# Optimization experiments

Hardware: AMD Instinct MI355X
Metric: run time of the kernel (lower is better)

## Reference

```python
import jax, jax.numpy as jnp
import numpy as np

N = 100000
E = 1600000
EPS = 1e-5


def _bn(h, g, b):
    # BatchNorm1d in training mode: batch stats over dim 0 (biased variance)
    mu = h.mean(0)
    var = ((h - mu) ** 2).mean(0)
    return g * (h - mu) * jax.lax.rsqrt(var + EPS) + b


def setup_inputs() -> dict:
    key = jax.random.key(0)

    def nrm(i, shape, scale=1.0):
        return jax.random.normal(jax.random.fold_in(key, i), shape, jnp.float32) * scale

    inp = {
        "x": nrm(0, (N, 1)),
        "edge_attr": nrm(1, (E, 2)),
        "edge_index": jax.random.randint(jax.random.fold_in(key, 2), (2, E), 0, N),
        "dir_edge_index": jax.random.randint(jax.random.fold_in(key, 3), (2, E), 0, N),
        "prop_edge_index": jax.random.randint(jax.random.fold_in(key, 4), (2, E), 0, N),
    }
    k = [10]

    def lin(name, fan_in, fan_out):
        inp[name] = nrm(k[0], (fan_in, fan_out), 1.0 / float(np.sqrt(fan_in)))
        k[0] += 1

    def bnp(prefix, c):
        inp[prefix + "_g"] = jnp.ones((c,), jnp.float32)
        inp[prefix + "_b"] = jnp.zeros((c,), jnp.float32)

    lin("c1_ws", 1, 2); lin("c1_wn", 1, 2); lin("c1_we", 2, 2); bnp("c1", 2)
    lin("d1_ws", 3, 4); lin("d1_wn", 3, 4); bnp("d1", 4)
    lin("c2_ws", 5, 6); lin("c2_wn", 5, 6); lin("c2_we", 2, 6); bnp("c2", 6)
    lin("d2_ws", 7, 8); lin("d2_wn", 7, 8); bnp("d2", 8)
    lin("c3_ws", 9, 10); lin("c3_wn", 9, 10); lin("c3_we", 2, 10); bnp("c3", 10)
    lin("d3_ws", 11, 12); lin("d3_wn", 11, 12); bnp("d3", 12)
    lin("pw1", 13, 8); inp["pb1"] = jnp.zeros((8,), jnp.float32); bnp("p1", 8)
    lin("pw2", 8, 4); inp["pb2"] = jnp.zeros((4,), jnp.float32); bnp("p2", 4)
    lin("pw3", 4, 1); inp["pb3"] = jnp.zeros((1,), jnp.float32)
    lin("ew1", 28, 14); inp["eb1"] = jnp.zeros((14,), jnp.float32); bnp("e1", 14)
    lin("ew2", 14, 1); inp["eb2"] = jnp.zeros((1,), jnp.float32)
    return inp


def reference(x, edge_attr, edge_index, dir_edge_index, prop_edge_index,
              c1_ws, c1_wn, c1_we, c1_g, c1_b,
              d1_ws, d1_wn, d1_g, d1_b,
              c2_ws, c2_wn, c2_we, c2_g, c2_b,
              d2_ws, d2_wn, d2_g, d2_b,
              c3_ws, c3_wn, c3_we, c3_g, c3_b,
              d3_ws, d3_wn, d3_g, d3_b,
              pw1, pb1, p1_g, p1_b, pw2, pb2, p2_g, p2_b, pw3, pb3,
              ew1, eb1, e1_g, e1_b, ew2, eb2):
    n = x.shape[0]
    src, dst = edge_index[0], edge_index[1]        # x_j = x[src], x_i = x[dst]
    psrc, pdst = prop_edge_index[0], prop_edge_index[1]

    def flexconv(h, ws, wn, we, g, b):
        m = jax.nn.relu(_bn(h[dst] @ ws + edge_attr @ we + h[src] @ wn, g, b))
        agg = jax.ops.segment_sum(m, dst, num_segments=n)
        return jnp.concatenate([h[:, :1], agg], axis=1)

    def edgeinter(h, ws, wn, g, b):
        m = jax.nn.relu(_bn(h[pdst] @ ws + h[psrc] @ wn, g, b))
        agg = jax.ops.segment_sum(m, pdst, num_segments=n)
        return jnp.concatenate([h[:, :1], agg], axis=1)

    out = flexconv(x, c1_ws, c1_wn, c1_we, c1_g, c1_b)      # [N,3]
    out = edgeinter(out, d1_ws, d1_wn, d1_g, d1_b)          # [N,5]
    out = flexconv(out, c2_ws, c2_wn, c2_we, c2_g, c2_b)    # [N,7]
    out = edgeinter(out, d2_ws, d2_wn, d2_g, d2_b)          # [N,9]
    out = flexconv(out, c3_ws, c3_wn, c3_we, c3_g, c3_b)    # [N,11]
    out = edgeinter(out, d3_ws, d3_wn, d3_g, d3_b)          # [N,13]

    h = _bn(jax.nn.relu(out @ pw1 + pb1), p1_g, p1_b)
    h = _bn(jax.nn.relu(h @ pw2 + pb2), p2_g, p2_b)
    power = jax.nn.sigmoid(1.5 * (h @ pw3 + pb3))           # [N,1]

    dsrc, ddst = dir_edge_index[0], dir_edge_index[1]
    f = jnp.concatenate([out[ddst], power[ddst], out[dsrc], power[dsrc]], axis=1)  # [E,28]
    e = _bn(jax.nn.relu(f @ ew1 + eb1), e1_g, e1_b)
    direction = jax.nn.sigmoid(1.5 * (e @ ew2 + eb2))       # [E,1]
    return power, direction
```

## Files before the change

kernel.cpp:

```cpp
#include <hip/hip_runtime.h>
#include <hip/hip_fp16.h>
#include <math.h>

static constexpr int BLK = 256;
static constexpr float BN_EPS = 1e-5f;

__device__ __forceinline__ float sigmoid15(float z) {
    return 1.0f / (1.0f + expf(-1.5f * z));
}

__device__ __forceinline__ unsigned pack_ea(float2 v) {
    unsigned hx = __half_as_ushort(__float2half_rn(v.x));
    unsigned hy = __half_as_ushort(__float2half_rn(v.y));
    return hx | (hy << 16);
}
__device__ __forceinline__ float2 unpack_ea(unsigned u) {
    return make_float2(__half2float(__ushort_as_half((unsigned short)(u & 0xffffu))),
                       __half2float(__ushort_as_half((unsigned short)(u >> 16))));
}

template<int C>
__device__ __forceinline__ void block_stats_reduce(float (&s)[C], float (&ss)[C],
                                                   double* __restrict__ stats)
{
    #pragma unroll
    for (int j = 0; j < C; ++j) {
        #pragma unroll
        for (int o = 32; o > 0; o >>= 1) {
            s[j]  += __shfl_down(s[j],  o, 64);
            ss[j] += __shfl_down(ss[j], o, 64);
        }
    }
    __shared__ float red[2][C][BLK / 64];
    const int wave = threadIdx.x >> 6, lane = threadIdx.x & 63;
    if (lane == 0) {
        #pragma unroll
        for (int j = 0; j < C; ++j) { red[0][j][wave] = s[j]; red[1][j][wave] = ss[j]; }
    }
    __syncthreads();
    if (threadIdx.x < C) {
        const int j = threadIdx.x;
        float a = 0.f, b = 0.f;
        #pragma unroll
        for (int w = 0; w < BLK / 64; ++w) { a += red[0][j][w]; b += red[1][j][w]; }
        atomicAdd(&stats[j],      (double)a);
        atomicAdd(&stats[16 + j], (double)b);
    }
}

template<int C>
__device__ __forceinline__ void bn_coefs(const double* __restrict__ stats,
                                         const float* __restrict__ g, const float* __restrict__ b,
                                         double invE, float (&sc)[C], float (&bb)[C])
{
    #pragma unroll
    for (int j = 0; j < C; ++j) {
        const double mu  = stats[j] * invE;
        const double var = stats[16 + j] * invE - mu * mu;
        const float inv = rsqrtf((float)(var + (double)BN_EPS));
        const float gg = g[j];
        sc[j] = gg * inv;
        bb[j] = b[j] - (float)mu * gg * inv;
    }
}


__global__ __launch_bounds__(BLK) void init_kernel(int* __restrict__ deg, double* __restrict__ stats,
                                                   int* __restrict__ rowstart, int n2, int total)
{
    const int i = blockIdx.x * blockDim.x + threadIdx.x;
    if (i < n2) deg[i] = 0;
    if (i < 288) stats[i] = 0.0;
    if (i == 0) rowstart[n2] = total;
}

__global__ __launch_bounds__(BLK) void hist_kernel(const int* __restrict__ edst,
                                                   const int* __restrict__ pdst,
                                                   int* __restrict__ deg, int N, int E)
{
    const int stride = gridDim.x * blockDim.x;
    for (int e = blockIdx.x * blockDim.x + threadIdx.x; e < E; e += stride) {
        atomicAdd(&deg[edst[e]], 1);
        atomicAdd(&deg[N + pdst[e]], 1);
    }
}

__global__ __launch_bounds__(256) void scan1_kernel(const int* __restrict__ deg,
                                                    int* __restrict__ rowstart,
                                                    int* __restrict__ partials, int n2)
{
    __shared__ int lds[256];
    const int tid = threadIdx.x;
    const int base = blockIdx.x * 1024 + tid * 4;
    int v[4]; int loc = 0;
    #pragma unroll
    for (int r = 0; r < 4; ++r) { v[r] = (base + r < n2) ? deg[base + r] : 0; loc += v[r]; }
    lds[tid] = loc; __syncthreads();
    #pragma unroll
    for (int off = 1; off < 256; off <<= 1) {
        int t = (tid >= off) ? lds[tid - off] : 0;
        __syncthreads();
        lds[tid] += t;
        __syncthreads();
    }
    int excl = lds[tid] - loc;
    int run = excl;
    #pragma unroll
    for (int r = 0; r < 4; ++r) {
        if (base + r < n2) rowstart[base + r] = run;
        run += v[r];
    }
    if (tid == 255) partials[blockIdx.x] = lds[255];
}

__global__ __launch_bounds__(256) void scan2_kernel(int* __restrict__ partials, int n)
{
    __shared__ int lds[256];
    const int tid = threadIdx.x;
    const int base = tid * 4;
    int v[4]; int loc = 0;
    #pragma unroll
    for (int r = 0; r < 4; ++r) { v[r] = (base + r < n) ? partials[base + r] : 0; loc += v[r]; }
    lds[tid] = loc; __syncthreads();
    #pragma unroll
    for (int off = 1; off < 256; off <<= 1) {
        int t = (tid >= off) ? lds[tid - off] : 0;
        __syncthreads();
        lds[tid] += t;
        __syncthreads();
    }
    int excl = lds[tid] - loc;
    int run = excl;
    #pragma unroll
    for (int r = 0; r < 4; ++r) {
        if (base + r < n) partials[base + r] = run;
        run += v[r];
    }
}

__global__ __launch_bounds__(BLK) void scan3_kernel(int* __restrict__ rowstart,
                                                    int* __restrict__ cursor,
                                                    const int* __restrict__ partials, int n2)
{
    const int i = blockIdx.x * blockDim.x + threadIdx.x;
    if (i >= n2) return;
    const int v = rowstart[i] + partials[i >> 10];
    rowstart[i] = v;
    cursor[i] = v;
}

__global__ __launch_bounds__(BLK) void fill_kernel(
    const int* __restrict__ esrc, const int* __restrict__ edst,
    const int* __restrict__ psrc, const int* __restrict__ pdst,
    const float* __restrict__ ea,
    int* __restrict__ cursor, uint2* __restrict__ csr_e,
    unsigned int* __restrict__ csr_psrc, int N, int E)
{
    const int stride = gridDim.x * blockDim.x;
    for (int e = blockIdx.x * blockDim.x + threadIdx.x; e < E; e += stride) {
        const int d = edst[e];
        const float2 eav = ((const float2*)ea)[e];
        const int pos = atomicAdd(&cursor[d], 1);
        csr_e[pos] = make_uint2((unsigned)esrc[e], pack_ea(eav));
        const int p = pdst[e];
        const int pos2 = atomicAdd(&cursor[N + p], 1);
        csr_psrc[pos2 - E] = (unsigned)psrc[e];
    }
}


template<int CIN, int COUT>
__global__ __launch_bounds__(BLK) void projQ_kernel(
    const float* __restrict__ x, const float* __restrict__ agg_in,
    const float* __restrict__ wn, float* __restrict__ Q, int n)
{
    constexpr int PAD = (COUT + 3) & ~3;
    __shared__ float swn[CIN * COUT];
    for (int i = threadIdx.x; i < CIN * COUT; i += blockDim.x) swn[i] = wn[i];
    __syncthreads();
    const int i = blockIdx.x * blockDim.x + threadIdx.x;
    if (i >= n) return;
    float h[CIN];
    h[0] = x[i];
    #pragma unroll
    for (int k = 1; k < CIN; ++k) h[k] = agg_in[(size_t)i * (CIN - 1) + (k - 1)];
    #pragma unroll
    for (int j = 0; j < COUT; ++j) {
        float q = 0.f;
        #pragma unroll
        for (int k = 0; k < CIN; ++k) q = fmaf(h[k], swn[k * COUT + j], q);
        Q[(size_t)i * PAD + j] = q;
    }
}

template<int CIN, int COUT, bool HASEA>
__global__ __launch_bounds__(BLK) void node_stats_kernel(
    const int* __restrict__ rowstart,
    const uint2* __restrict__ csr_e, const unsigned int* __restrict__ csr_psrc,
    const float* __restrict__ x, const float* __restrict__ agg_in,
    const float* __restrict__ ws, const float* __restrict__ Q,
    const float* __restrict__ we,
    double* __restrict__ stats, int N, int base, int koff)
{
    constexpr int PAD = (COUT + 3) & ~3;
    __shared__ float sws[CIN * COUT];
    for (int i = threadIdx.x; i < CIN * COUT; i += blockDim.x) sws[i] = ws[i];
    __syncthreads();
    float we0[COUT], we1[COUT];
    if constexpr (HASEA) {
        #pragma unroll
        for (int j = 0; j < COUT; ++j) { we0[j] = we[j]; we1[j] = we[COUT + j]; }
    }
    float s[COUT], ss[COUT];
    #pragma unroll
    for (int j = 0; j < COUT; ++j) { s[j] = 0.f; ss[j] = 0.f; }
    const int t = blockIdx.x * blockDim.x + threadIdx.x;
    const int i = t >> 2, quad = t & 3;
    if (i < N) {
        float h[CIN];
        h[0] = x[i];
        #pragma unroll
        for (int k = 1; k < CIN; ++k) h[k] = agg_in[(size_t)i * (CIN - 1) + (k - 1)];
        float pp[COUT];
        #pragma unroll
        for (int j = 0; j < COUT; ++j) {
            float p = 0.f;
            #pragma unroll
            for (int k = 0; k < CIN; ++k) p = fmaf(h[k], sws[k * COUT + j], p);
            pp[j] = p;
        }
        const int k0 = rowstart[base + i], k1 = rowstart[base + i + 1];
        for (int k = k0 + quad; k < k1; k += 4) {
            unsigned sn;
            float2 eav;
            if constexpr (HASEA) {
                const uint2 ce = csr_e[k];
                sn = ce.x; eav = unpack_ea(ce.y);
            } else {
                sn = csr_psrc[k - koff];
            }
            #pragma unroll
            for (int j = 0; j < COUT; ++j) {
                float m = pp[j] + Q[(size_t)sn * PAD + j];
                if constexpr (HASEA) m = fmaf(eav.x, we0[j], fmaf(eav.y, we1[j], m));
                s[j] += m; ss[j] = fmaf(m, m, ss[j]);
            }
        }
    }
    block_stats_reduce<COUT>(s, ss, stats);
}

template<int CIN, int COUT, bool HASEA>
__global__ __launch_bounds__(BLK) void node_agg_kernel(
    const int* __restrict__ rowstart,
    const uint2* __restrict__ csr_e, const unsigned int* __restrict__ csr_psrc,
    const float* __restrict__ x, const float* __restrict__ agg_in,
    const float* __restrict__ ws, const float* __restrict__ Q,
    const float* __restrict__ we,
    const float* __restrict__ g, const float* __restrict__ b,
    const double* __restrict__ stats,
    float* __restrict__ agg_out, int N, int base, int koff, float invE)
{
    constexpr int PAD = (COUT + 3) & ~3;
    __shared__ float sws[CIN * COUT];
    for (int i = threadIdx.x; i < CIN * COUT; i += blockDim.x) sws[i] = ws[i];
    __syncthreads();
    const int t = blockIdx.x * blockDim.x + threadIdx.x;
    const int i = t >> 2, quad = t & 3;
    if (i >= N) return;
    float we0[COUT], we1[COUT];
    if constexpr (HASEA) {
        #pragma unroll
        for (int j = 0; j < COUT; ++j) { we0[j] = we[j]; we1[j] = we[COUT + j]; }
    }
    float sc[COUT], bb[COUT];
    bn_coefs<COUT>(stats, g, b, (double)invE, sc, bb);
    float h[CIN];
    h[0] = x[i];
    #pragma unroll
    for (int k = 1; k < CIN; ++k) h[k] = agg_in[(size_t)i * (CIN - 1) + (k - 1)];
    float pp[COUT], acc[COUT];
    #pragma unroll
    for (int j = 0; j < COUT; ++j) {
        float p = 0.f;
        #pragma unroll
        for (int k = 0; k < CIN; ++k) p = fmaf(h[k], sws[k * COUT + j], p);
        pp[j] = p; acc[j] = 0.f;
    }
    const int k0 = rowstart[base + i], k1 = rowstart[base + i + 1];
    for (int k = k0 + quad; k < k1; k += 4) {
        unsigned sn;
        float2 eav;
        if constexpr (HASEA) {
            const uint2 ce = csr_e[k];
            sn = ce.x; eav = unpack_ea(ce.y);
        } else {
            sn = csr_psrc[k - koff];
        }
        #pragma unroll
        for (int j = 0; j < COUT; ++j) {
            float m = pp[j] + Q[(size_t)sn * PAD + j];
            if constexpr (HASEA) m = fmaf(eav.x, we0[j], fmaf(eav.y, we1[j], m));
            acc[j] += fmaxf(fmaf(sc[j], m, bb[j]), 0.f);
        }
    }
    #pragma unroll
    for (int j = 0; j < COUT; ++j) {
        acc[j] += __shfl_xor(acc[j], 1, 64);
        acc[j] += __shfl_xor(acc[j], 2, 64);
    }
    if (quad == 0) {
        #pragma unroll
        for (int j = 0; j < COUT; ++j) agg_out[(size_t)i * COUT + j] = acc[j];
    }
}


__global__ __launch_bounds__(BLK) void zero_stats_kernel(double* __restrict__ stats, int n)
{
    int i = blockIdx.x * blockDim.x + threadIdx.x;
    if (i < n) stats[i] = 0.0;
}

template<int CIN, int COUT>
__global__ __launch_bounds__(BLK) void projPQ_kernel(
    const float* __restrict__ x, const float* __restrict__ agg_in,
    const float* __restrict__ ws, const float* __restrict__ wn,
    float* __restrict__ P, float* __restrict__ Q, float* __restrict__ agg_out, int n)
{
    __shared__ float sws[CIN * COUT], swn[CIN * COUT];
    for (int i = threadIdx.x; i < CIN * COUT; i += blockDim.x) { sws[i] = ws[i]; swn[i] = wn[i]; }
    __syncthreads();
    const int i = blockIdx.x * blockDim.x + threadIdx.x;
    if (i >= n) return;
    float h[CIN];
    h[0] = x[i];
    #pragma unroll
    for (int k = 1; k < CIN; ++k) h[k] = agg_in[(size_t)i * (CIN - 1) + (k - 1)];
    #pragma unroll
    for (int j = 0; j < COUT; ++j) {
        float p = 0.f, q = 0.f;
        #pragma unroll
        for (int k = 0; k < CIN; ++k) {
            p = fmaf(h[k], sws[k * COUT + j], p);
            q = fmaf(h[k], swn[k * COUT + j], q);
        }
        P[(size_t)i * COUT + j] = p;
        Q[(size_t)i * COUT + j] = q;
        agg_out[(size_t)i * COUT + j] = 0.f;
    }
}

template<int COUT, bool HASEA>
__global__ __launch_bounds__(BLK) void edge_stats_kernel(
    const int* __restrict__ esrc, const int* __restrict__ edst,
    const float* __restrict__ P,  const float* __restrict__ Q,
    const float* __restrict__ ea, const float* __restrict__ we,
    double* __restrict__ stats, int E)
{
    float we0[COUT], we1[COUT];
    if constexpr (HASEA) {
        #pragma unroll
        for (int j = 0; j < COUT; ++j) { we0[j] = we[j]; we1[j] = we[COUT + j]; }
    }
    float s[COUT], ss[COUT];
    #pragma unroll
    for (int j = 0; j < COUT; ++j) { s[j] = 0.f; ss[j] = 0.f; }
    const int stride = gridDim.x * blockDim.x;
    for (int e = blockIdx.x * blockDim.x + threadIdx.x; e < E; e += stride) {
        const int d = edst[e], sn = esrc[e];
        float2 eav = make_float2(0.f, 0.f);
        if constexpr (HASEA) eav = ((const float2* __restrict__)ea)[e];
        #pragma unroll
        for (int j = 0; j < COUT; ++j) {
            float m = P[(size_t)d * COUT + j] + Q[(size_t)sn * COUT + j];
            if constexpr (HASEA) m += eav.x * we0[j] + eav.y * we1[j];
            s[j] += m; ss[j] = fmaf(m, m, ss[j]);
        }
    }
    block_stats_reduce<COUT>(s, ss, stats);
}

template<int COUT, bool HASEA>
__global__ __launch_bounds__(BLK) void edge_scatter_kernel(
    const int* __restrict__ esrc, const int* __restrict__ edst,
    const float* __restrict__ P,  const float* __restrict__ Q,
    const float* __restrict__ ea, const float* __restrict__ we,
    const float* __restrict__ g,  const float* __restrict__ b,
    const double* __restrict__ stats,
    float* __restrict__ agg_out, int E)
{
    float we0[COUT], we1[COUT], sc[COUT], bb[COUT];
    #pragma unroll
    for (int j = 0; j < COUT; ++j) {
        if constexpr (HASEA) { we0[j] = we[j]; we1[j] = we[COUT + j]; }
    }
    bn_coefs<COUT>(stats, g, b, 1.0 / (double)E, sc, bb);
    const int stride = gridDim.x * blockDim.x;
    for (int e = blockIdx.x * blockDim.x + threadIdx.x; e < E; e += stride) {
        const int d = edst[e], sn = esrc[e];
        float2 eav = make_float2(0.f, 0.f);
        if constexpr (HASEA) eav = ((const float2* __restrict__)ea)[e];
        #pragma unroll
        for (int j = 0; j < COUT; ++j) {
            float m = P[(size_t)d * COUT + j] + Q[(size_t)sn * COUT + j];
            if constexpr (HASEA) m += eav.x * we0[j] + eav.y * we1[j];
            const float y = fmaxf(fmaf(sc[j], m, bb[j]), 0.f);
            if (y > 0.f) unsafeAtomicAdd(&agg_out[(size_t)d * COUT + j], y);
        }
    }
}


__global__ __launch_bounds__(BLK) void mlp1_kernel(
    const float* __restrict__ x, const float* __restrict__ agg6,
    const float* __restrict__ pw1, const float* __restrict__ pb1,
    float* __restrict__ t1, double* __restrict__ stats, int n)
{
    __shared__ float w[13 * 8];
    __shared__ float bsh[8];
    for (int i = threadIdx.x; i < 13 * 8; i += blockDim.x) w[i] = pw1[i];
    if (threadIdx.x < 8) bsh[threadIdx.x] = pb1[threadIdx.x];
    __syncthreads();
    const int i = blockIdx.x * blockDim.x + threadIdx.x;
    float s[8], ss[8];
    #pragma unroll
    for (int j = 0; j < 8; ++j) { s[j] = 0.f; ss[j] = 0.f; }
    if (i < n) {
        float h[13];
        h[0] = x[i];
        #pragma unroll
        for (int k = 0; k < 12; ++k) h[k + 1] = agg6[(size_t)i * 12 + k];
        #pragma unroll
        for (int j = 0; j < 8; ++j) {
            float t = bsh[j];
            #pragma unroll
            for (int k = 0; k < 13; ++k) t = fmaf(h[k], w[k * 8 + j], t);
            t = fmaxf(t, 0.f);
            t1[(size_t)i * 8 + j] = t;
            s[j] = t; ss[j] = t * t;
        }
    }
    block_stats_reduce<8>(s, ss, stats);
}

__global__ __launch_bounds__(BLK) void mlp2_kernel(
    const float* __restrict__ t1,
    const float* __restrict__ p1g, const float* __restrict__ p1b,
    const float* __restrict__ pw2, const float* __restrict__ pb2,
    const double* __restrict__ stats1,
    float* __restrict__ t2, double* __restrict__ stats2, int n)
{
    float sc[8], bb[8];
    bn_coefs<8>(stats1, p1g, p1b, 1.0 / (double)n, sc, bb);
    const int i = blockIdx.x * blockDim.x + threadIdx.x;
    float s[4], ss[4];
    #pragma unroll
    for (int j = 0; j < 4; ++j) { s[j] = 0.f; ss[j] = 0.f; }
    if (i < n) {
        float u[8];
        #pragma unroll
        for (int j = 0; j < 8; ++j) u[j] = fmaf(sc[j], t1[(size_t)i * 8 + j], bb[j]);
        #pragma unroll
        for (int j2 = 0; j2 < 4; ++j2) {
            float t = pb2[j2];
            #pragma unroll
            for (int j = 0; j < 8; ++j) t = fmaf(u[j], pw2[j * 4 + j2], t);
            t = fmaxf(t, 0.f);
            t2[(size_t)i * 4 + j2] = t;
            s[j2] = t; ss[j2] = t * t;
        }
    }
    block_stats_reduce<4>(s, ss, stats2);
}

__global__ __launch_bounds__(BLK) void mlp3_kernel(
    const float* __restrict__ t2,
    const float* __restrict__ p2g, const float* __restrict__ p2b,
    const float* __restrict__ pw3, const float* __restrict__ pb3,
    const float* __restrict__ x, const float* __restrict__ agg6,
    const float* __restrict__ ew1, const float* __restrict__ eb1,
    const double* __restrict__ stats2,
    float* __restrict__ power_out, float* __restrict__ A, float* __restrict__ B,
    int n, int astride)
{
    __shared__ float w1[28 * 14];
    for (int i = threadIdx.x; i < 28 * 14; i += blockDim.x) w1[i] = ew1[i];
    __syncthreads();
    float sc[4], bb[4];
    bn_coefs<4>(stats2, p2g, p2b, 1.0 / (double)n, sc, bb);
    const int i = blockIdx.x * blockDim.x + threadIdx.x;
    if (i >= n) return;
    float z = pb3[0];
    #pragma unroll
    for (int j = 0; j < 4; ++j) z = fmaf(fmaf(sc[j], t2[(size_t)i * 4 + j], bb[j]), pw3[j], z);
    const float pw = sigmoid15(z);
    power_out[i] = pw;
    float h[14];
    h[0] = x[i];
    #pragma unroll
    for (int k = 0; k < 12; ++k) h[k + 1] = agg6[(size_t)i * 12 + k];
    h[13] = pw;
    #pragma unroll
    for (int c = 0; c < 14; ++c) {
        float a = eb1[c], b2 = 0.f;
        #pragma unroll
        for (int k = 0; k < 14; ++k) {
            a  = fmaf(h[k], w1[k * 14 + c], a);
            b2 = fmaf(h[k], w1[(14 + k) * 14 + c], b2);
        }
        A[(size_t)i * astride + c] = a;
        B[(size_t)i * astride + c] = b2;
    }
}

__global__ __launch_bounds__(BLK) void ehead_stats_kernel(
    const int* __restrict__ dsrc, const int* __restrict__ ddst,
    const float* __restrict__ A, const float* __restrict__ B,
    double* __restrict__ stats, int E, int astride)
{
    float s[14], ss[14];
    #pragma unroll
    for (int j = 0; j < 14; ++j) { s[j] = 0.f; ss[j] = 0.f; }
    const int stride = gridDim.x * blockDim.x;
    for (int e = blockIdx.x * blockDim.x + threadIdx.x; e < E; e += stride) {
        const int dd = ddst[e], ds = dsrc[e];
        #pragma unroll
        for (int c = 0; c < 14; ++c) {
            const float r = fmaxf(A[(size_t)dd * astride + c] + B[(size_t)ds * astride + c], 0.f);
            s[c] += r; ss[c] = fmaf(r, r, ss[c]);
        }
    }
    block_stats_reduce<14>(s, ss, stats);
}

__global__ __launch_bounds__(BLK) void ehead_final_kernel(
    const int* __restrict__ dsrc, const int* __restrict__ ddst,
    const float* __restrict__ A, const float* __restrict__ B,
    const float* __restrict__ e1g, const float* __restrict__ e1b,
    const float* __restrict__ ew2, const float* __restrict__ eb2,
    const double* __restrict__ stats, float* __restrict__ dir_out, int E, int astride)
{
    float sc[14];
    float off = eb2[0];
    const double invE = 1.0 / (double)E;
    #pragma unroll
    for (int c = 0; c < 14; ++c) {
        const double mu  = stats[c] * invE;
        const double var = stats[16 + c] * invE - mu * mu;
        const float inv = rsqrtf((float)(var + (double)BN_EPS));
        const float gi = e1g[c] * inv;
        sc[c] = gi * ew2[c];
        off += (e1b[c] - (float)mu * gi) * ew2[c];
    }
    const int stride = gridDim.x * blockDim.x;
    for (int e = blockIdx.x * blockDim.x + threadIdx.x; e < E; e += stride) {
        const int dd = ddst[e], ds = dsrc[e];
        float z = off;
        #pragma unroll
        for (int c = 0; c < 14; ++c) {
            const float r = fmaxf(A[(size_t)dd * astride + c] + B[(size_t)ds * astride + c], 0.f);
            z = fmaf(r, sc[c], z);
        }
        dir_out[e] = sigmoid15(z);
    }
}


extern "C" void kernel_launch(void* const* d_in, const int* in_sizes, int n_in,
                              void* d_out, int out_size, void* d_ws, size_t ws_size,
                              hipStream_t stream)
{
    const float* x    = (const float*)d_in[0];
    const float* ea   = (const float*)d_in[1];
    const int*   eidx = (const int*)d_in[2];
    const int*   didx = (const int*)d_in[3];
    const int*   pidx = (const int*)d_in[4];
    const float *c1_ws=(const float*)d_in[5],  *c1_wn=(const float*)d_in[6],  *c1_we=(const float*)d_in[7],  *c1_g=(const float*)d_in[8],  *c1_b=(const float*)d_in[9];
    const float *d1_ws=(const float*)d_in[10], *d1_wn=(const float*)d_in[11], *d1_g=(const float*)d_in[12], *d1_b=(const float*)d_in[13];
    const float *c2_ws=(const float*)d_in[14], *c2_wn=(const float*)d_in[15], *c2_we=(const float*)d_in[16], *c2_g=(const float*)d_in[17], *c2_b=(const float*)d_in[18];
    const float *d2_ws=(const float*)d_in[19], *d2_wn=(const float*)d_in[20], *d2_g=(const float*)d_in[21], *d2_b=(const float*)d_in[22];
    const float *c3_ws=(const float*)d_in[23], *c3_wn=(const float*)d_in[24], *c3_we=(const float*)d_in[25], *c3_g=(const float*)d_in[26], *c3_b=(const float*)d_in[27];
    const float *d3_ws=(const float*)d_in[28], *d3_wn=(const float*)d_in[29], *d3_g=(const float*)d_in[30], *d3_b=(const float*)d_in[31];
    const float *pw1=(const float*)d_in[32], *pb1=(const float*)d_in[33], *p1_g=(const float*)d_in[34], *p1_b=(const float*)d_in[35];
    const float *pw2=(const float*)d_in[36], *pb2=(const float*)d_in[37], *p2_g=(const float*)d_in[38], *p2_b=(const float*)d_in[39];
    const float *pw3=(const float*)d_in[40], *pb3=(const float*)d_in[41];
    const float *ew1=(const float*)d_in[42], *eb1=(const float*)d_in[43], *e1_g=(const float*)d_in[44], *e1_b=(const float*)d_in[45];
    const float *ew2=(const float*)d_in[46], *eb2=(const float*)d_in[47];

    const int N = in_sizes[0];
    const int E = in_sizes[2] / 2;
    const int n2 = 2 * N;
    const int *esrc = eidx,     *edst = eidx + E;
    const int *dsrc = didx,     *ddst = didx + E;
    const int *psrc = pidx,     *pdst = pidx + E;

    float* power_out = (float*)d_out;
    float* dir_out   = power_out + N;

    const int gN  = (N + BLK - 1) / BLK;
    const int g2  = (n2 + BLK - 1) / BLK;
    const int g4  = ((size_t)4 * N + BLK - 1) / BLK;
    const int gE  = 1024;
    const int gEf = (E + BLK - 1) / BLK;
    const float invE = 1.0f / (float)E;

    const size_t abFloats = (size_t)32 * N;
    const size_t csreBytes = ((size_t)8 * E > 4 * abFloats) ? (size_t)8 * E : 4 * abFloats;
    const size_t need_csr = 4096
        + sizeof(float) * ((size_t)N * 12
                         + (size_t)N * 12
                         + (size_t)N * 12)
        + csreBytes
        + sizeof(unsigned int) * (size_t)E
        + sizeof(int) * ((size_t)n2 + 2)
        + sizeof(int) * (size_t)n2
        + sizeof(int) * 1024;

    double* stats = (double*)d_ws;

    if (ws_size >= need_csr) {
        float* fws  = (float*)((char*)d_ws + 4096);
        float* Q    = fws;                fws += (size_t)N * 12;
        float* aggA = fws;                fws += (size_t)N * 12;
        float* aggB = fws;                fws += (size_t)N * 12;
        uint2* csr_e = (uint2*)fws;
        unsigned int* csr_psrc = (unsigned int*)((char*)csr_e + csreBytes);
        int* rowstart = (int*)(csr_psrc + E);
        int* cursor   = rowstart + (n2 + 2);
        int* deg      = cursor;
        int* partials = cursor + n2;
        float* t1   = aggA;
        float* t2   = aggA + (size_t)N * 8;
        float* Abuf = (float*)csr_e;
        float* Bbuf = Abuf + (size_t)N * 16;

        const int nparts = (n2 + 1023) / 1024;

        init_kernel<<<g2, BLK, 0, stream>>>(deg, stats, rowstart, n2, 2 * E);
        hist_kernel<<<gEf, BLK, 0, stream>>>(edst, pdst, deg, N, E);
        scan1_kernel<<<nparts, 256, 0, stream>>>(deg, rowstart, partials, n2);
        scan2_kernel<<<1, 256, 0, stream>>>(partials, nparts);
        scan3_kernel<<<g2, BLK, 0, stream>>>(rowstart, cursor, partials, n2);
        fill_kernel<<<gEf, BLK, 0, stream>>>(esrc, edst, psrc, pdst, ea, cursor, csr_e, csr_psrc, N, E);

        projQ_kernel<1, 2><<<gN, BLK, 0, stream>>>(x, nullptr, c1_wn, Q, N);
        node_stats_kernel<1, 2, true><<<g4, BLK, 0, stream>>>(rowstart, csr_e, csr_psrc, x, nullptr, c1_ws, Q, c1_we, stats + 0, N, 0, 0);
        node_agg_kernel<1, 2, true><<<g4, BLK, 0, stream>>>(rowstart, csr_e, csr_psrc, x, nullptr, c1_ws, Q, c1_we, c1_g, c1_b, stats + 0, aggA, N, 0, 0, invE);
        projQ_kernel<3, 4><<<gN, BLK, 0, stream>>>(x, aggA, d1_wn, Q, N);
        node_stats_kernel<3, 4, false><<<g4, BLK, 0, stream>>>(rowstart, csr_e, csr_psrc, x, aggA, d1_ws, Q, nullptr, stats + 32, N, N, E);
        node_agg_kernel<3, 4, false><<<g4, BLK, 0, stream>>>(rowstart, csr_e, csr_psrc, x, aggA, d1_ws, Q, nullptr, d1_g, d1_b, stats + 32, aggB, N, N, E, invE);
        projQ_kernel<5, 6><<<gN, BLK, 0, stream>>>(x, aggB, c2_wn, Q, N);
        node_stats_kernel<5, 6, true><<<g4, BLK, 0, stream>>>(rowstart, csr_e, csr_psrc, x, aggB, c2_ws, Q, c2_we, stats + 64, N, 0, 0);
        node_agg_kernel<5, 6, true><<<g4, BLK, 0, stream>>>(rowstart, csr_e, csr_psrc, x, aggB, c2_ws, Q, c2_we, c2_g, c2_b, stats + 64, aggA, N, 0, 0, invE);
        projQ_kernel<7, 8><<<gN, BLK, 0, stream>>>(x, aggA, d2_wn, Q, N);
        node_stats_kernel<7, 8, false><<<g4, BLK, 0, stream>>>(rowstart, csr_e, csr_psrc, x, aggA, d2_ws, Q, nullptr, stats + 96, N, N, E);
        node_agg_kernel<7, 8, false><<<g4, BLK, 0, stream>>>(rowstart, csr_e, csr_psrc, x, aggA, d2_ws, Q, nullptr, d2_g, d2_b, stats + 96, aggB, N, N, E, invE);
        projQ_kernel<9, 10><<<gN, BLK, 0, stream>>>(x, aggB, c3_wn, Q, N);
        node_stats_kernel<9, 10, true><<<g4, BLK, 0, stream>>>(rowstart, csr_e, csr_psrc, x, aggB, c3_ws, Q, c3_we, stats + 128, N, 0, 0);
        node_agg_kernel<9, 10, true><<<g4, BLK, 0, stream>>>(rowstart, csr_e, csr_psrc, x, aggB, c3_ws, Q, c3_we, c3_g, c3_b, stats + 128, aggA, N, 0, 0, invE);
        projQ_kernel<11, 12><<<gN, BLK, 0, stream>>>(x, aggA, d3_wn, Q, N);
        node_stats_kernel<11, 12, false><<<g4, BLK, 0, stream>>>(rowstart, csr_e, csr_psrc, x, aggA, d3_ws, Q, nullptr, stats + 160, N, N, E);
        node_agg_kernel<11, 12, false><<<g4, BLK, 0, stream>>>(rowstart, csr_e, csr_psrc, x, aggA, d3_ws, Q, nullptr, d3_g, d3_b, stats + 160, aggB, N, N, E, invE);

        mlp1_kernel<<<gN, BLK, 0, stream>>>(x, aggB, pw1, pb1, t1, stats + 192, N);
        mlp2_kernel<<<gN, BLK, 0, stream>>>(t1, p1_g, p1_b, pw2, pb2, stats + 192, t2, stats + 224, N);
        mlp3_kernel<<<gN, BLK, 0, stream>>>(t2, p2_g, p2_b, pw3, pb3, x, aggB, ew1, eb1, stats + 224,
                                            power_out, Abuf, Bbuf, N, 16);
        ehead_stats_kernel<<<gE, BLK, 0, stream>>>(dsrc, ddst, Abuf, Bbuf, stats + 256, E, 16);
        ehead_final_kernel<<<gEf, BLK, 0, stream>>>(dsrc, ddst, Abuf, Bbuf, e1_g, e1_b, ew2, eb2,
                                                    stats + 256, dir_out, E, 16);
    } else {
        float* fws  = (float*)((char*)d_ws + 4096);
        float* P    = fws;                fws += (size_t)N * 14;
        float* Q    = fws;                fws += (size_t)N * 14;
        float* aggA = fws;                fws += (size_t)N * 12;
        float* aggB = fws;                fws += (size_t)N * 12;
        float* t1   = aggA;
        float* t2   = aggA + (size_t)N * 8;
        float* Abuf = P;
        float* Bbuf = Q;

        zero_stats_kernel<<<2, BLK, 0, stream>>>(stats, 288);

        projPQ_kernel<1, 2><<<gN, BLK, 0, stream>>>(x, nullptr, c1_ws, c1_wn, P, Q, aggA, N);
        edge_stats_kernel<2, true><<<gE, BLK, 0, stream>>>(esrc, edst, P, Q, ea, c1_we, stats + 0, E);
        edge_scatter_kernel<2, true><<<gE, BLK, 0, stream>>>(esrc, edst, P, Q, ea, c1_we, c1_g, c1_b, stats + 0, aggA, E);

        projPQ_kernel<3, 4><<<gN, BLK, 0, stream>>>(x, aggA, d1_ws, d1_wn, P, Q, aggB, N);
        edge_stats_kernel<4, false><<<gE, BLK, 0, stream>>>(psrc, pdst, P, Q, nullptr, nullptr, stats + 32, E);
        edge_scatter_kernel<4, false><<<gE, BLK, 0, stream>>>(psrc, pdst, P, Q, nullptr, nullptr, d1_g, d1_b, stats + 32, aggB, E);

        projPQ_kernel<5, 6><<<gN, BLK, 0, stream>>>(x, aggB, c2_ws, c2_wn, P, Q, aggA, N);
        edge_stats_kernel<6, true><<<gE, BLK, 0, stream>>>(esrc, edst, P, Q, ea, c2_we, stats + 64, E);
        edge_scatter_kernel<6, true><<<gE, BLK, 0, stream>>>(esrc, edst, P, Q, ea, c2_we, c2_g, c2_b, stats + 64, aggA, E);

        projPQ_kernel<7, 8><<<gN, BLK, 0, stream>>>(x, aggA, d2_ws, d2_wn, P, Q, aggB, N);
        edge_stats_kernel<8, false><<<gE, BLK, 0, stream>>>(psrc, pdst, P, Q, nullptr, nullptr, stats + 96, E);
        edge_scatter_kernel<8, false><<<gE, BLK, 0, stream>>>(psrc, pdst, P, Q, nullptr, nullptr, d2_g, d2_b, stats + 96, aggB, E);

        projPQ_kernel<9, 10><<<gN, BLK, 0, stream>>>(x, aggB, c3_ws, c3_wn, P, Q, aggA, N);
        edge_stats_kernel<10, true><<<gE, BLK, 0, stream>>>(esrc, edst, P, Q, ea, c3_we, stats + 128, E);
        edge_scatter_kernel<10, true><<<gE, BLK, 0, stream>>>(esrc, edst, P, Q, ea, c3_we, c3_g, c3_b, stats + 128, aggA, E);

        projPQ_kernel<11, 12><<<gN, BLK, 0, stream>>>(x, aggA, d3_ws, d3_wn, P, Q, aggB, N);
        edge_stats_kernel<12, false><<<gE, BLK, 0, stream>>>(psrc, pdst, P, Q, nullptr, nullptr, stats + 160, E);
        edge_scatter_kernel<12, false><<<gE, BLK, 0, stream>>>(psrc, pdst, P, Q, nullptr, nullptr, d3_g, d3_b, stats + 160, aggB, E);

        mlp1_kernel<<<gN, BLK, 0, stream>>>(x, aggB, pw1, pb1, t1, stats + 192, N);
        mlp2_kernel<<<gN, BLK, 0, stream>>>(t1, p1_g, p1_b, pw2, pb2, stats + 192, t2, stats + 224, N);
        mlp3_kernel<<<gN, BLK, 0, stream>>>(t2, p2_g, p2_b, pw3, pb3, x, aggB, ew1, eb1, stats + 224,
                                            power_out, Abuf, Bbuf, N, 14);
        ehead_stats_kernel<<<gE, BLK, 0, stream>>>(dsrc, ddst, Abuf, Bbuf, stats + 256, E, 14);
        ehead_final_kernel<<<gE, BLK, 0, stream>>>(dsrc, ddst, Abuf, Bbuf, e1_g, e1_b, ew2, eb2,
                                                   stats + 256, dir_out, E, 14);
    }
}
```

Measured before the change: 1.091 ms.

## Partition CSR build by destination range and fuse next-layer Q projection into aggregation

The histogram and fill kernels now split blocks into eight groups, each handling one quarter of the node range for either the edge or the propagation graph. The aim is better atomic locality on the degree and cursor arrays, at the cost of every group re-reading the full index arrays. Separately, node_agg_kernel now computes the next layer's neighbor projection Q from its freshly reduced aggregate and writes it to a second buffer. This removes five projQ launches and their re-read of the aggregate, but needs an extra N*12 float workspace buffer.

```diff
diff --git a/kernel.cpp b/kernel.cpp
--- a/kernel.cpp
+++ b/kernel.cpp
@@ -78,10 +78,22 @@
                                                    const int* __restrict__ pdst,
                                                    int* __restrict__ deg, int N, int E)
 {
-    const int stride = gridDim.x * blockDim.x;
-    for (int e = blockIdx.x * blockDim.x + threadIdx.x; e < E; e += stride) {
-        atomicAdd(&deg[edst[e]], 1);
-        atomicAdd(&deg[N + pdst[e]], 1);
+    const int grp = blockIdx.x & 7;
+    const int bg  = blockIdx.x >> 3;
+    const int gstride = (gridDim.x >> 3) * blockDim.x;
+    if (grp < 4) {
+        const int lo = (int)((size_t)N * grp / 4), hi = (int)((size_t)N * (grp + 1) / 4);
+        for (int e = bg * blockDim.x + threadIdx.x; e < E; e += gstride) {
+            const int d = edst[e];
+            if (d >= lo && d < hi) atomicAdd(&deg[d], 1);
+        }
+    } else {
+        const int gg = grp - 4;
+        const int lo = (int)((size_t)N * gg / 4), hi = (int)((size_t)N * (gg + 1) / 4);
+        for (int e = bg * blockDim.x + threadIdx.x; e < E; e += gstride) {
+            const int p = pdst[e];
+            if (p >= lo && p < hi) atomicAdd(&deg[N + p], 1);
+        }
     }
 }
 
@@ -156,15 +168,29 @@
     int* __restrict__ cursor, uint2* __restrict__ csr_e,
     unsigned int* __restrict__ csr_psrc, int N, int E)
 {
-    const int stride = gridDim.x * blockDim.x;
-    for (int e = blockIdx.x * blockDim.x + threadIdx.x; e < E; e += stride) {
-        const int d = edst[e];
-        const float2 eav = ((const float2*)ea)[e];
-        const int pos = atomicAdd(&cursor[d], 1);
-        csr_e[pos] = make_uint2((unsigned)esrc[e], pack_ea(eav));
-        const int p = pdst[e];
-        const int pos2 = atomicAdd(&cursor[N + p], 1);
-        csr_psrc[pos2 - E] = (unsigned)psrc[e];
+    const int grp = blockIdx.x & 7;
+    const int bg  = blockIdx.x >> 3;
+    const int gstride = (gridDim.x >> 3) * blockDim.x;
+    if (grp < 4) {
+        const int lo = (int)((size_t)N * grp / 4), hi = (int)((size_t)N * (grp + 1) / 4);
+        for (int e = bg * blockDim.x + threadIdx.x; e < E; e += gstride) {
+            const int d = edst[e];
+            if (d >= lo && d < hi) {
+                const float2 eav = ((const float2*)ea)[e];
+                const int pos = atomicAdd(&cursor[d], 1);
+                csr_e[pos] = make_uint2((unsigned)esrc[e], pack_ea(eav));
+            }
+        }
+    } else {
+        const int gg = grp - 4;
+        const int lo = (int)((size_t)N * gg / 4), hi = (int)((size_t)N * (gg + 1) / 4);
+        for (int e = bg * blockDim.x + threadIdx.x; e < E; e += gstride) {
+            const int p = pdst[e];
+            if (p >= lo && p < hi) {
+                const int pos2 = atomicAdd(&cursor[N + p], 1);
+                csr_psrc[pos2 - E] = (unsigned)psrc[e];
+            }
+        }
     }
 }
 
@@ -250,7 +276,7 @@
     block_stats_reduce<COUT>(s, ss, stats);
 }
 
-template<int CIN, int COUT, bool HASEA>
+template<int CIN, int COUT, bool HASEA, int CIN2, int COUT2>
 __global__ __launch_bounds__(BLK) void node_agg_kernel(
     const int* __restrict__ rowstart,
     const uint2* __restrict__ csr_e, const unsigned int* __restrict__ csr_psrc,
@@ -259,11 +285,19 @@
     const float* __restrict__ we,
     const float* __restrict__ g, const float* __restrict__ b,
     const double* __restrict__ stats,
-    float* __restrict__ agg_out, int N, int base, int koff, float invE)
+    float* __restrict__ agg_out,
+    const float* __restrict__ wn2, float* __restrict__ Qout,
+    int N, int base, int koff, float invE)
 {
     constexpr int PAD = (COUT + 3) & ~3;
+    constexpr bool FUSEQ = (COUT2 > 0);
+    constexpr int W2 = FUSEQ ? CIN2 * COUT2 : 1;
     __shared__ float sws[CIN * COUT];
+    __shared__ float swn2[W2];
     for (int i = threadIdx.x; i < CIN * COUT; i += blockDim.x) sws[i] = ws[i];
+    if constexpr (FUSEQ) {
+        for (int i = threadIdx.x; i < W2; i += blockDim.x) swn2[i] = wn2[i];
+    }
     __syncthreads();
     const int t = blockIdx.x * blockDim.x + threadIdx.x;
     const int i = t >> 2, quad = t & 3;
@@ -312,6 +346,17 @@
     if (quad == 0) {
         #pragma unroll
         for (int j = 0; j < COUT; ++j) agg_out[(size_t)i * COUT + j] = acc[j];
+        if constexpr (FUSEQ) {
+            constexpr int PAD2 = (COUT2 + 3) & ~3;
+            #pragma unroll
+            for (int j2 = 0; j2 < COUT2; ++j2) {
+                float q = h[0] * swn2[j2];
+                #pragma unroll
+                for (int k = 0; k < COUT; ++k)
+                    q = fmaf(acc[k], swn2[(k + 1) * COUT2 + j2], q);
+                Qout[(size_t)i * PAD2 + j2] = q;
+            }
+        }
     }
 }
 
@@ -603,12 +648,14 @@
     const int g4  = ((size_t)4 * N + BLK - 1) / BLK;
     const int gE  = 1024;
     const int gEf = (E + BLK - 1) / BLK;
+    const int gX  = 8 * 160;
     const float invE = 1.0f / (float)E;
 
     const size_t abFloats = (size_t)32 * N;
     const size_t csreBytes = ((size_t)8 * E > 4 * abFloats) ? (size_t)8 * E : 4 * abFloats;
     const size_t need_csr = 4096
         + sizeof(float) * ((size_t)N * 12
+                         + (size_t)N * 12
                          + (size_t)N * 12
                          + (size_t)N * 12)
         + csreBytes
@@ -621,7 +668,8 @@
 
     if (ws_size >= need_csr) {
         float* fws  = (float*)((char*)d_ws + 4096);
-        float* Q    = fws;                fws += (size_t)N * 12;
+        float* Qa   = fws;                fws += (size_t)N * 12;
+        float* Qb   = fws;                fws += (size_t)N * 12;
         float* aggA = fws;                fws += (size_t)N * 12;
         float* aggB = fws;                fws += (size_t)N * 12;
         uint2* csr_e = (uint2*)fws;
@@ -638,30 +686,25 @@
         const int nparts = (n2 + 1023) / 1024;
 
         init_kernel<<<g2, BLK, 0, stream>>>(deg, stats, rowstart, n2, 2 * E);
-        hist_kernel<<<gEf, BLK, 0, stream>>>(edst, pdst, deg, N, E);
+        hist_kernel<<<gX, BLK, 0, stream>>>(edst, pdst, deg, N, E);
         scan1_kernel<<<nparts, 256, 0, stream>>>(deg, rowstart, partials, n2);
         scan2_kernel<<<1, 256, 0, stream>>>(partials, nparts);
         scan3_kernel<<<g2, BLK, 0, stream>>>(rowstart, cursor, partials, n2);
-        fill_kernel<<<gEf, BLK, 0, stream>>>(esrc, edst, psrc, pdst, ea, cursor, csr_e, csr_psrc, N, E);
-
-        projQ_kernel<1, 2><<<gN, BLK, 0, stream>>>(x, nullptr, c1_wn, Q, N);
-        node_stats_kernel<1, 2, true><<<g4, BLK, 0, stream>>>(rowstart, csr_e, csr_psrc, x, nullptr, c1_ws, Q, c1_we, stats + 0, N, 0, 0);
-        node_agg_kernel<1, 2, true><<<g4, BLK, 0, stream>>>(rowstart, csr_e, csr_psrc, x, nullptr, c1_ws, Q, c1_we, c1_g, c1_b, stats + 0, aggA, N, 0, 0, invE);
-        projQ_kernel<3, 4><<<gN, BLK, 0, stream>>>(x, aggA, d1_wn, Q, N);
-        node_stats_kernel<3, 4, false><<<g4, BLK, 0, stream>>>(rowstart, csr_e, csr_psrc, x, aggA, d1_ws, Q, nullptr, stats + 32, N, N, E);
-        node_agg_kernel<3, 4, false><<<g4, BLK, 0, stream>>>(rowstart, csr_e, csr_psrc, x, aggA, d1_ws, Q, nullptr, d1_g, d1_b, stats + 32, aggB, N, N, E, invE);
-        projQ_kernel<5, 6><<<gN, BLK, 0, stream>>>(x, aggB, c2_wn, Q, N);
-        node_stats_kernel<5, 6, true><<<g4, BLK, 0, stream>>>(rowstart, csr_e, csr_psrc, x, aggB, c2_ws, Q, c2_we, stats + 64, N, 0, 0);
-        node_agg_kernel<5, 6, true><<<g4, BLK, 0, stream>>>(rowstart, csr_e, csr_psrc, x, aggB, c2_ws, Q, c2_we, c2_g, c2_b, stats + 64, aggA, N, 0, 0, invE);
-        projQ_kernel<7, 8><<<gN, BLK, 0, stream>>>(x, aggA, d2_wn, Q, N);
-        node_stats_kernel<7, 8, false><<<g4, BLK, 0, stream>>>(rowstart, csr_e, csr_psrc, x, aggA, d2_ws, Q, nullptr, stats + 96, N, N, E);
-        node_agg_kernel<7, 8, false><<<g4, BLK, 0, stream>>>(rowstart, csr_e, csr_psrc, x, aggA, d2_ws, Q, nullptr, d2_g, d2_b, stats + 96, aggB, N, N, E, invE);
-        projQ_kernel<9, 10><<<gN, BLK, 0, stream>>>(x, aggB, c3_wn, Q, N);
-        node_stats_kernel<9, 10, true><<<g4, BLK, 0, stream>>>(rowstart, csr_e, csr_psrc, x, aggB, c3_ws, Q, c3_we, stats + 128, N, 0, 0);
-        node_agg_kernel<9, 10, true><<<g4, BLK, 0, stream>>>(rowstart, csr_e, csr_psrc, x, aggB, c3_ws, Q, c3_we, c3_g, c3_b, stats + 128, aggA, N, 0, 0, invE);
-        projQ_kernel<11, 12><<<gN, BLK, 0, stream>>>(x, aggA, d3_wn, Q, N);
-        node_stats_kernel<11, 12, false><<<g4, BLK, 0, stream>>>(rowstart, csr_e, csr_psrc, x, aggA, d3_ws, Q, nullptr, stats + 160, N, N, E);
-        node_agg_kernel<11, 12, false><<<g4, BLK, 0, stream>>>(rowstart, csr_e, csr_psrc, x, aggA, d3_ws, Q, nullptr, d3_g, d3_b, stats + 160, aggB, N, N, E, invE);
+        fill_kernel<<<gX, BLK, 0, stream>>>(esrc, edst, psrc, pdst, ea, cursor, csr_e, csr_psrc, N, E);
+
+        projQ_kernel<1, 2><<<gN, BLK, 0, stream>>>(x, nullptr, c1_wn, Qa, N);
+        node_stats_kernel<1, 2, true><<<g4, BLK, 0, stream>>>(rowstart, csr_e, csr_psrc, x, nullptr, c1_ws, Qa, c1_we, stats + 0, N, 0, 0);
+        node_agg_kernel<1, 2, true, 3, 4><<<g4, BLK, 0, stream>>>(rowstart, csr_e, csr_psrc, x, nullptr, c1_ws, Qa, c1_we, c1_g, c1_b, stats + 0, aggA, d1_wn, Qb, N, 0, 0, invE);
+        node_stats_kernel<3, 4, false><<<g4, BLK, 0, stream>>>(rowstart, csr_e, csr_psrc, x, aggA, d1_ws, Qb, nullptr, stats + 32, N, N, E);
+        node_agg_kernel<3, 4, false, 5, 6><<<g4, BLK, 0, stream>>>(rowstart, csr_e, csr_psrc, x, aggA, d1_ws, Qb, nullptr, d1_g, d1_b, stats + 32, aggB, c2_wn, Qa, N, N, E, invE);
+        node_stats_kernel<5, 6, true><<<g4, BLK, 0, stream>>>(rowstart, csr_e, csr_psrc, x, aggB, c2_ws, Qa, c2_we, stats + 64, N, 0, 0);
+        node_agg_kernel<5, 6, true, 7, 8><<<g4, BLK, 0, stream>>>(rowstart, csr_e, csr_psrc, x, aggB, c2_ws, Qa, c2_we, c2_g, c2_b, stats + 64, aggA, d2_wn, Qb, N, 0, 0, invE);
+        node_stats_kernel<7, 8, false><<<g4, BLK, 0, stream>>>(rowstart, csr_e, csr_psrc, x, aggA, d2_ws, Qb, nullptr, stats + 96, N, N, E);
+        node_agg_kernel<7, 8, false, 9, 10><<<g4, BLK, 0, stream>>>(rowstart, csr_e, csr_psrc, x, aggA, d2_ws, Qb, nullptr, d2_g, d2_b, stats + 96, aggB, c3_wn, Qa, N, N, E, invE);
+        node_stats_kernel<9, 10, true><<<g4, BLK, 0, stream>>>(rowstart, csr_e, csr_psrc, x, aggB, c3_ws, Qa, c3_we, stats + 128, N, 0, 0);
+        node_agg_kernel<9, 10, true, 11, 12><<<g4, BLK, 0, stream>>>(rowstart, csr_e, csr_psrc, x, aggB, c3_ws, Qa, c3_we, c3_g, c3_b, stats + 128, aggA, d3_wn, Qb, N, 0, 0, invE);
+        node_stats_kernel<11, 12, false><<<g4, BLK, 0, stream>>>(rowstart, csr_e, csr_psrc, x, aggA, d3_ws, Qb, nullptr, stats + 160, N, N, E);
+        node_agg_kernel<11, 12, false, 0, 0><<<g4, BLK, 0, stream>>>(rowstart, csr_e, csr_psrc, x, aggA, d3_ws, Qb, nullptr, d3_g, d3_b, stats + 160, aggB, nullptr, nullptr, N, N, E, invE);
 
         mlp1_kernel<<<gN, BLK, 0, stream>>>(x, aggB, pw1, pb1, t1, stats + 192, N);
         mlp2_kernel<<<gN, BLK, 0, stream>>>(t1, p1_g, p1_b, pw2, pb2, stats + 192, t2, stats + 224, N);
```

Result: faster. 952.1 us (-12.7%).
